# Optimization experiments

Measured on AMD Instinct MI355X. Metric: run time of the kernel, lower is better.

Reference implementation:

```python
import jax, jax.numpy as jnp
import numpy as np

TEMPERATURE = 0.1  # InfoNCE default
K_POS, K_NEG = 5, 10


def _l2norm(x, eps):
    return x / jnp.maximum(jnp.linalg.norm(x, axis=-1, keepdims=True), eps)


def setup_inputs() -> dict:
    key = jax.random.key(0)
    k1, k2 = jax.random.split(key)
    anchor = jax.random.normal(k1, (4096, 512), dtype=jnp.float32)
    sample = jax.random.normal(k2, (4096, 512), dtype=jnp.float32)
    return {"anchor": anchor, "sample": sample}


def reference(anchor, sample):
    N = anchor.shape[0]
    # Pairwise cosine similarity (torch.cosine_similarity eps=1e-8), computed
    a = _l2norm(anchor, 1e-8)
    sim = a @ a.T  # (N, N)

    # topk largest=True (5 nearest) and largest=False (10 farthest)
    _, pos_idx = jax.lax.top_k(sim, K_POS)    # (N, 5)
    _, neg_idx = jax.lax.top_k(-sim, K_NEG)   # (N, 10), ascending sim

    # Faithful replication of the original gather/repeat pattern:
    # query = sample.repeat(5, 1) -> tiling (index i maps to sample[i % N])
    query = jnp.tile(sample, (K_POS, 1))                          # (5N, d)
    pos = sample[pos_idx.reshape(-1)]                             # (5N, d) anchor-major
    neg = sample[neg_idx.reshape(-1)].reshape(N, K_NEG, -1)       # (N, 10, d)
    neg = jnp.repeat(neg, K_POS, axis=0)                          # (5N, 10, d)

    # InfoNCE (negative_mode='paired'): F.normalize (eps=1e-12) then logits.
    q = _l2norm(query, 1e-12)
    p = _l2norm(pos, 1e-12)
    n = _l2norm(neg, 1e-12)
    pos_logit = jnp.sum(q * p, axis=1, keepdims=True)             # (5N, 1)
    neg_logits = jnp.einsum('bd,bkd->bk', q, n)                   # (5N, 10)
    logits = jnp.concatenate([pos_logit, neg_logits], axis=1) / TEMPERATURE
    # cross_entropy with labels == 0, mean reduction
    loss = -jnp.mean(jax.nn.log_softmax(logits, axis=1)[:, 0])
    return loss
```

## Files before the change

### kernel.cpp

```cpp
#include <hip/hip_runtime.h>
#include <math.h>

#define N 4096
#define D 512
#define KPOS 5
#define KNEG 10
#define NB 32
#define NPAIR (NB * (NB - 1) / 2)
#define NJOB 1024

typedef short s16x8 __attribute__((ext_vector_type(8)));
typedef unsigned short u16x8 __attribute__((ext_vector_type(8)));
typedef float f32x4 __attribute__((ext_vector_type(4)));

__device__ __forceinline__ unsigned short f2bf(float x) {
    unsigned u = __float_as_uint(x);
    unsigned r = (u + 0x7FFFu + ((u >> 16) & 1u)) >> 16;
    return (unsigned short)r;
}
__device__ __forceinline__ float bf2f(unsigned short b) {
    return __uint_as_float(((unsigned)b) << 16);
}
__device__ __forceinline__ unsigned short mapbf(float x) {
    const unsigned short h = f2bf(x);
    return h ^ ((h & 0x8000u) ? 0xFFFFu : 0x8000u);
}
__device__ __forceinline__ unsigned umax_(unsigned a, unsigned b) { return a > b ? a : b; }
__device__ __forceinline__ unsigned umin_(unsigned a, unsigned b) { return a < b ? a : b; }

__global__ __launch_bounds__(256) void norm_kernel(const float* __restrict__ anchor,
                                                   const float* __restrict__ sample,
                                                   unsigned short* __restrict__ Abf,
                                                   unsigned short* __restrict__ s_norm) {
    const int wave = threadIdx.x >> 6, lane = threadIdx.x & 63;
    const int row = blockIdx.x * 4 + wave;
    const bool is_anchor = row < N;
    const float* in = is_anchor ? anchor + (size_t)row * D
                                : sample + (size_t)(row - N) * D;
    const float eps = is_anchor ? 1e-8f : 1e-12f;

    float v[8];
    float ss = 0.f;
#pragma unroll
    for (int e = 0; e < 8; ++e) {
        v[e] = in[lane + 64 * e];
        ss = fmaf(v[e], v[e], ss);
    }
#pragma unroll
    for (int off = 32; off > 0; off >>= 1) ss += __shfl_xor(ss, off);
    const float denom = fmaxf(sqrtf(ss), eps);

    unsigned short* out = is_anchor ? Abf + (size_t)row * D
                                    : s_norm + (size_t)(row - N) * D;
#pragma unroll
    for (int e = 0; e < 8; ++e) out[lane + 64 * e] = f2bf(v[e] / denom);
}

#define ATILE (128 * 64)
#define BTILE (64 * 64)

__device__ __forceinline__ void stage_ab(const unsigned short* __restrict__ A,
                                         unsigned short* As, unsigned short* Bs,
                                         int rowA, int colB, int kl, int t) {
#pragma unroll
    for (int i = 0; i < 4; ++i) {
        const int c = i * 256 + t;
        const int r = c >> 3;
        const int ke = ((c & 7) ^ (r & 7)) * 8;
        __builtin_amdgcn_global_load_lds(
            (const __attribute__((address_space(1))) void*)(A + (size_t)(rowA + r) * D + kl + ke),
            (__attribute__((address_space(3))) void*)(As + c * 8), 16, 0, 0);
    }
#pragma unroll
    for (int i = 0; i < 2; ++i) {
        const int c = i * 256 + t;
        const int r = c >> 3;
        const int ke = ((c & 7) ^ (r & 7)) * 8;
        __builtin_amdgcn_global_load_lds(
            (const __attribute__((address_space(1))) void*)(A + (size_t)(colB + r) * D + kl + ke),
            (__attribute__((address_space(3))) void*)(Bs + c * 8), 16, 0, 0);
    }
}

__global__ __launch_bounds__(256) void gemm_bf16(const unsigned short* __restrict__ Abf,
                                                 unsigned short* __restrict__ C) {
    const int q = (blockIdx.x % 8) * (NJOB / 8) + blockIdx.x / 8;

    int bi, bj, h;
    if (q < 2 * NPAIR) {
        const int op = q >> 1;
        h = q & 1;
        bi = (int)(31.5f - sqrtf(31.5f * 31.5f - 2.f * (float)op));
        while (31 * bi - bi * (bi - 1) / 2 > op) --bi;
        while (31 * (bi + 1) - (bi + 1) * bi / 2 <= op) ++bi;
        bj = bi + 1 + (op - (31 * bi - bi * (bi - 1) / 2));
    } else {
        const int d = q - 2 * NPAIR;
        bi = bj = d >> 1;
        h = d & 1;
    }

    __shared__ __align__(16) unsigned short As[2 * ATILE];
    __shared__ __align__(16) unsigned short Bs[2 * BTILE];

    const int t = threadIdx.x;
    const int l = t & 63;
    const int w = t >> 6;
    const int wr = w >> 1, wc = w & 1;
    const int rowA = bi * 128;
    const int colB = bj * 128 + h * 64;
    const int lrow = l & 15, lgrp = l >> 4;

    f32x4 acc[4][2];
#pragma unroll
    for (int m = 0; m < 4; ++m)
#pragma unroll
        for (int n = 0; n < 2; ++n) acc[m][n] = (f32x4){0.f, 0.f, 0.f, 0.f};

    stage_ab(Abf, As, Bs, rowA, colB, 0, t);
    __syncthreads();

    for (int kc = 0; kc < 8; ++kc) {
        const int cur = kc & 1;
        if (kc < 7)
            stage_ab(Abf, As + (cur ^ 1) * ATILE, Bs + (cur ^ 1) * BTILE,
                     rowA, colB, (kc + 1) * 64, t);

        const char* AsB = (const char*)(As + cur * ATILE);
        const char* BsB = (const char*)(Bs + cur * BTILE);
#pragma unroll
        for (int kk = 0; kk < 2; ++kk) {
            s16x8 af[4], bfr[2];
#pragma unroll
            for (int m = 0; m < 4; ++m) {
                const int row = wr * 64 + m * 16 + lrow;
                af[m] = *(const s16x8*)(AsB + row * 128 + (((kk * 4 + lgrp) ^ (row & 7)) * 16));
            }
#pragma unroll
            for (int n = 0; n < 2; ++n) {
                const int row = wc * 32 + n * 16 + lrow;
                bfr[n] = *(const s16x8*)(BsB + row * 128 + (((kk * 4 + lgrp) ^ (row & 7)) * 16));
            }
#pragma unroll
            for (int m = 0; m < 4; ++m)
#pragma unroll
                for (int n = 0; n < 2; ++n)
                    acc[m][n] = __builtin_amdgcn_mfma_f32_16x16x32_bf16(af[m], bfr[n], acc[m][n], 0, 0, 0);
        }
        __syncthreads();
    }

#pragma unroll
    for (int m = 0; m < 4; ++m) {
#pragma unroll
        for (int n = 0; n < 2; ++n) {
            const int col = colB + wc * 32 + n * 16 + lrow;
            const int row0 = rowA + wr * 64 + m * 16 + lgrp * 4;
#pragma unroll
            for (int j = 0; j < 4; ++j)
                C[(size_t)(row0 + j) * N + col] = mapbf(acc[m][n][j]);
        }
    }
    if (bi != bj) {
#pragma unroll
        for (int m = 0; m < 4; ++m) {
#pragma unroll
            for (int n = 0; n < 2; ++n) {
                const int col = colB + wc * 32 + n * 16 + lrow;
                const int row0 = rowA + wr * 64 + m * 16 + lgrp * 4;
                ushort4 pk;
                pk.x = mapbf(acc[m][n][0]);
                pk.y = mapbf(acc[m][n][1]);
                pk.z = mapbf(acc[m][n][2]);
                pk.w = mapbf(acc[m][n][3]);
                *(ushort4*)&C[(size_t)col * N + row0] = pk;
            }
        }
    }
}

__device__ __forceinline__ void ins_top(unsigned* tk, unsigned c) {
#pragma unroll
    for (int q = 0; q < KPOS - 1; ++q) {
        const unsigned x = umax_(tk[q], c);
        c = umin_(tk[q], c);
        tk[q] = x;
    }
    tk[KPOS - 1] = umax_(tk[KPOS - 1], c);
}
__device__ __forceinline__ void ins_bot(unsigned* bk, unsigned c) {
#pragma unroll
    for (int q = 0; q < KNEG - 1; ++q) {
        const unsigned x = umin_(bk[q], c);
        c = umax_(bk[q], c);
        bk[q] = x;
    }
    bk[KNEG - 1] = umin_(bk[KNEG - 1], c);
}
__device__ __forceinline__ void scan8(const unsigned short* __restrict__ s,
                                      int lane, int e, unsigned* tk, unsigned* bk) {
    const int base = 8 * (lane + 64 * e);
    const u16x8 v8 = *(const u16x8*)&s[base];
#pragma unroll
    for (int j = 0; j < 8; ++j) {
        const unsigned kv = ((unsigned)v8[j]) << 16;
        const int idx = base + j;
        ins_top(tk, kv | (unsigned)(idx ^ 0xFFF));
        ins_bot(bk, kv | (unsigned)idx);
    }
}

__global__ __launch_bounds__(256) void topk_kernel(const unsigned short* __restrict__ sim,
                                                   int* __restrict__ pos_idx,
                                                   int* __restrict__ neg_idx) {
    const int w = threadIdx.x >> 6, l = threadIdx.x & 63;
    const int row = blockIdx.x * 4 + w;
    const unsigned short* s = sim + (size_t)row * N;

    unsigned tkA[KPOS], bkA[KNEG], tkB[KPOS], bkB[KNEG];
#pragma unroll
    for (int q = 0; q < KPOS; ++q) { tkA[q] = 0u; tkB[q] = 0u; }
#pragma unroll
    for (int q = 0; q < KNEG; ++q) { bkA[q] = 0xFFFFFFFFu; bkB[q] = 0xFFFFFFFFu; }

#pragma unroll
    for (int ee = 0; ee < 4; ++ee) {
        scan8(s, l, 2 * ee, tkA, bkA);
        scan8(s, l, 2 * ee + 1, tkB, bkB);
    }
#pragma unroll
    for (int q = 0; q < KPOS; ++q) ins_top(tkA, tkB[q]);
#pragma unroll
    for (int q = 0; q < KNEG; ++q) ins_bot(bkA, bkB[q]);

#pragma unroll
    for (int it = 0; it < KPOS; ++it) {
        unsigned m = tkA[0];
#pragma unroll
        for (int off = 32; off > 0; off >>= 1) m = umax_(m, (unsigned)__shfl_xor((int)m, off));
        if (l == 0) pos_idx[row * KPOS + it] = (int)((m & 0xFFFu) ^ 0xFFFu);
        if (tkA[0] == m) {
#pragma unroll
            for (int q = 0; q < KPOS - 1; ++q) tkA[q] = tkA[q + 1];
            tkA[KPOS - 1] = 0u;
        }
    }
#pragma unroll
    for (int it = 0; it < KNEG; ++it) {
        unsigned m = bkA[0];
#pragma unroll
        for (int off = 32; off > 0; off >>= 1) m = umin_(m, (unsigned)__shfl_xor((int)m, off));
        if (l == 0) neg_idx[row * KNEG + it] = (int)(m & 0xFFFu);
        if (bkA[0] == m) {
#pragma unroll
            for (int q = 0; q < KNEG - 1; ++q) bkA[q] = bkA[q + 1];
            bkA[KNEG - 1] = 0xFFFFFFFFu;
        }
    }
}

__global__ __launch_bounds__(256) void loss_kernel(const unsigned short* __restrict__ s_norm,
                                                   const int* __restrict__ pos_idx,
                                                   const int* __restrict__ neg_idx,
                                                   float* __restrict__ partials) {
    __shared__ float wsum[4];
    const int wave = threadIdx.x >> 6, lane = threadIdx.x & 63;
    const int ia = blockIdx.x * 4 + wave;
    const int cc = lane & 15;
    const int g = lane >> 4;

    const int qbase = ia * KPOS;
    const int rowA = (qbase + ((cc < KPOS) ? cc : 0)) & (N - 1);
    int rowB;
    if (cc < KPOS)      rowB = pos_idx[qbase + cc];
    else if (cc < 15)   rowB = neg_idx[ia * KNEG + (cc - KPOS)];
    else                rowB = pos_idx[qbase];

    const unsigned short* pA = s_norm + (size_t)rowA * D + g * 8;
    const unsigned short* pB = s_norm + (size_t)rowB * D + g * 8;

    s16x8 a[16], b[16];
#pragma unroll
    for (int kk = 0; kk < 16; ++kk) {
        a[kk] = *(const s16x8*)(pA + kk * 32);
        b[kk] = *(const s16x8*)(pB + kk * 32);
    }
    __builtin_amdgcn_sched_barrier(0);
    asm volatile("" ::: "memory");

    f32x4 acc = (f32x4){0.f, 0.f, 0.f, 0.f};
#pragma unroll
    for (int kk = 0; kk < 16; ++kk)
        acc = __builtin_amdgcn_mfma_f32_16x16x32_bf16(a[kk], b[kk], acc, 0, 0, 0);

    float lsum = 0.f;
#pragma unroll
    for (int j = 0; j < 4; ++j) {
        const int p = g * 4 + j;
        const float logit = acc[j] * 10.f;
        const bool isneg = (cc >= KPOS) && (cc < 15);
        const bool ispos = (cc == p);
        float x = (ispos || isneg) ? logit : -__builtin_inff();
        float m = x;
#pragma unroll
        for (int off = 1; off < 16; off <<= 1) m = fmaxf(m, __shfl_xor(m, off));
        float e = (ispos || isneg) ? expf(logit - m) : 0.f;
        float sx = e;
#pragma unroll
        for (int off = 1; off < 16; off <<= 1) sx += __shfl_xor(sx, off);
        float l0 = ispos ? logit : 0.f;
#pragma unroll
        for (int off = 1; off < 16; off <<= 1) l0 += __shfl_xor(l0, off);
        if (p < KPOS && ispos) lsum += logf(sx) + m - l0;
    }

#pragma unroll
    for (int off = 32; off > 0; off >>= 1) lsum += __shfl_xor(lsum, off);
    if (lane == 0) wsum[wave] = lsum;
    __syncthreads();
    if (threadIdx.x == 0)
        partials[blockIdx.x] = wsum[0] + wsum[1] + wsum[2] + wsum[3];
}

__global__ __launch_bounds__(256) void reduce_kernel(const float* __restrict__ partials,
                                                     float* __restrict__ out) {
    __shared__ float wsum[4];
    const int wave = threadIdx.x >> 6, lane = threadIdx.x & 63;
    float s = partials[threadIdx.x] + partials[threadIdx.x + 256] +
              partials[threadIdx.x + 512] + partials[threadIdx.x + 768];
#pragma unroll
    for (int off = 32; off > 0; off >>= 1) s += __shfl_xor(s, off);
    if (lane == 0) wsum[wave] = s;
    __syncthreads();
    if (threadIdx.x == 0)
        *out = (wsum[0] + wsum[1] + wsum[2] + wsum[3]) * (1.0f / (float)(N * KPOS));
}

extern "C" void kernel_launch(void* const* d_in, const int* in_sizes, int n_in,
                              void* d_out, int out_size, void* d_ws, size_t ws_size,
                              hipStream_t stream) {
    const float* anchor = (const float*)d_in[0];
    const float* sample = (const float*)d_in[1];
    float* out = (float*)d_out;

    char* ws = (char*)d_ws;
    unsigned short* Abf    = (unsigned short*)ws;
    unsigned short* s_norm = (unsigned short*)(ws + (size_t)4 * 1024 * 1024);
    unsigned short* sim    = (unsigned short*)(ws + (size_t)8 * 1024 * 1024);
    int* pos_idx  = (int*)(ws + (size_t)40 * 1024 * 1024);
    int* neg_idx  = (int*)(ws + (size_t)40 * 1024 * 1024 + 128 * 1024);
    float* partials = (float*)(ws + (size_t)41 * 1024 * 1024);

    norm_kernel<<<2048, 256, 0, stream>>>(anchor, sample, Abf, s_norm);

    gemm_bf16<<<NJOB, 256, 0, stream>>>(Abf, sim);

    topk_kernel<<<N / 4, 256, 0, stream>>>(sim, pos_idx, neg_idx);

    loss_kernel<<<N / 4, 256, 0, stream>>>(s_norm, pos_idx, neg_idx, partials);

    reduce_kernel<<<1, 256, 0, stream>>>(partials, out);
}
```

Baseline: 71.01 us.

## Fuse top-k selection into loss kernel and vectorize normalization loads

Merges the top-k kernel and the loss kernel into one launch. Each wave finds its row's positive and negative indices with shuffles and hands them straight to the lanes that gather the sample rows, so the index arrays no longer go through global memory and one launch is removed. The normalization kernel also switches to float4 loads, ushort4 stores and a reciprocal multiply. The fused kernel holds more registers, which may reduce occupancy.

Measured after the change: 66.53 us. 6.3% less time.

```diff
diff --git a/kernel.cpp b/kernel.cpp
--- a/kernel.cpp
+++ b/kernel.cpp
@@ -39,21 +39,23 @@
                                 : sample + (size_t)(row - N) * D;
     const float eps = is_anchor ? 1e-8f : 1e-12f;
 
-    float v[8];
-    float ss = 0.f;
-#pragma unroll
-    for (int e = 0; e < 8; ++e) {
-        v[e] = in[lane + 64 * e];
-        ss = fmaf(v[e], v[e], ss);
-    }
+    const float4 v0 = *(const float4*)&in[lane * 4];
+    const float4 v1 = *(const float4*)&in[256 + lane * 4];
+    float ss = v0.x * v0.x + v0.y * v0.y + v0.z * v0.z + v0.w * v0.w
+             + v1.x * v1.x + v1.y * v1.y + v1.z * v1.z + v1.w * v1.w;
 #pragma unroll
     for (int off = 32; off > 0; off >>= 1) ss += __shfl_xor(ss, off);
-    const float denom = fmaxf(sqrtf(ss), eps);
+    const float inv = 1.0f / fmaxf(sqrtf(ss), eps);
 
     unsigned short* out = is_anchor ? Abf + (size_t)row * D
                                     : s_norm + (size_t)(row - N) * D;
-#pragma unroll
-    for (int e = 0; e < 8; ++e) out[lane + 64 * e] = f2bf(v[e] / denom);
+    ushort4 o0, o1;
+    o0.x = f2bf(v0.x * inv); o0.y = f2bf(v0.y * inv);
+    o0.z = f2bf(v0.z * inv); o0.w = f2bf(v0.w * inv);
+    o1.x = f2bf(v1.x * inv); o1.y = f2bf(v1.y * inv);
+    o1.z = f2bf(v1.z * inv); o1.w = f2bf(v1.w * inv);
+    *(ushort4*)&out[lane * 4] = o0;
+    *(ushort4*)&out[256 + lane * 4] = o1;
 }
 
 #define ATILE (128 * 64)
@@ -210,72 +212,59 @@
     }
 }
 
-__global__ __launch_bounds__(256) void topk_kernel(const unsigned short* __restrict__ sim,
-                                                   int* __restrict__ pos_idx,
-                                                   int* __restrict__ neg_idx) {
-    const int w = threadIdx.x >> 6, l = threadIdx.x & 63;
-    const int row = blockIdx.x * 4 + w;
-    const unsigned short* s = sim + (size_t)row * N;
-
-    unsigned tkA[KPOS], bkA[KNEG], tkB[KPOS], bkB[KNEG];
-#pragma unroll
-    for (int q = 0; q < KPOS; ++q) { tkA[q] = 0u; tkB[q] = 0u; }
-#pragma unroll
-    for (int q = 0; q < KNEG; ++q) { bkA[q] = 0xFFFFFFFFu; bkB[q] = 0xFFFFFFFFu; }
-
-#pragma unroll
-    for (int ee = 0; ee < 4; ++ee) {
-        scan8(s, l, 2 * ee, tkA, bkA);
-        scan8(s, l, 2 * ee + 1, tkB, bkB);
-    }
-#pragma unroll
-    for (int q = 0; q < KPOS; ++q) ins_top(tkA, tkB[q]);
-#pragma unroll
-    for (int q = 0; q < KNEG; ++q) ins_bot(bkA, bkB[q]);
-
-#pragma unroll
-    for (int it = 0; it < KPOS; ++it) {
-        unsigned m = tkA[0];
-#pragma unroll
-        for (int off = 32; off > 0; off >>= 1) m = umax_(m, (unsigned)__shfl_xor((int)m, off));
-        if (l == 0) pos_idx[row * KPOS + it] = (int)((m & 0xFFFu) ^ 0xFFFu);
-        if (tkA[0] == m) {
-#pragma unroll
-            for (int q = 0; q < KPOS - 1; ++q) tkA[q] = tkA[q + 1];
-            tkA[KPOS - 1] = 0u;
-        }
-    }
-#pragma unroll
-    for (int it = 0; it < KNEG; ++it) {
-        unsigned m = bkA[0];
-#pragma unroll
-        for (int off = 32; off > 0; off >>= 1) m = umin_(m, (unsigned)__shfl_xor((int)m, off));
-        if (l == 0) neg_idx[row * KNEG + it] = (int)(m & 0xFFFu);
-        if (bkA[0] == m) {
-#pragma unroll
-            for (int q = 0; q < KNEG - 1; ++q) bkA[q] = bkA[q + 1];
-            bkA[KNEG - 1] = 0xFFFFFFFFu;
-        }
-    }
-}
-
-__global__ __launch_bounds__(256) void loss_kernel(const unsigned short* __restrict__ s_norm,
-                                                   const int* __restrict__ pos_idx,
-                                                   const int* __restrict__ neg_idx,
-                                                   float* __restrict__ partials) {
+__global__ __launch_bounds__(256) void fused_topk_loss(const unsigned short* __restrict__ sim,
+                                                       const unsigned short* __restrict__ s_norm,
+                                                       float* __restrict__ partials) {
     __shared__ float wsum[4];
     const int wave = threadIdx.x >> 6, lane = threadIdx.x & 63;
     const int ia = blockIdx.x * 4 + wave;
+    const unsigned short* s = sim + (size_t)ia * N;
     const int cc = lane & 15;
     const int g = lane >> 4;
 
-    const int qbase = ia * KPOS;
-    const int rowA = (qbase + ((cc < KPOS) ? cc : 0)) & (N - 1);
-    int rowB;
-    if (cc < KPOS)      rowB = pos_idx[qbase + cc];
-    else if (cc < 15)   rowB = neg_idx[ia * KNEG + (cc - KPOS)];
-    else                rowB = pos_idx[qbase];
-
+    unsigned tkA[KPOS], bkA[KNEG], tkB[KPOS], bkB[KNEG];
+#pragma unroll
+    for (int q = 0; q < KPOS; ++q) { tkA[q] = 0u; tkB[q] = 0u; }
+#pragma unroll
+    for (int q = 0; q < KNEG; ++q) { bkA[q] = 0xFFFFFFFFu; bkB[q] = 0xFFFFFFFFu; }
+
+#pragma unroll
+    for (int ee = 0; ee < 4; ++ee) {
+        scan8(s, lane, 2 * ee, tkA, bkA);
+        scan8(s, lane, 2 * ee + 1, tkB, bkB);
+    }
+#pragma unroll
+    for (int q = 0; q < KPOS; ++q) ins_top(tkA, tkB[q]);
+#pragma unroll
+    for (int q = 0; q < KNEG; ++q) ins_bot(bkA, bkB[q]);
+
+    int rowB = 0;
+#pragma unroll
+    for (int it = 0; it < KPOS; ++it) {
+        unsigned m = tkA[0];
+#pragma unroll
+        for (int off = 32; off > 0; off >>= 1) m = umax_(m, (unsigned)__shfl_xor((int)m, off));
+        if (cc == it) rowB = (int)((m & 0xFFFu) ^ 0xFFFu);
+        if (tkA[0] == m) {
+#pragma unroll
+            for (int q = 0; q < KPOS - 1; ++q) tkA[q] = tkA[q + 1];
+            tkA[KPOS - 1] = 0u;
+        }
+    }
+#pragma unroll
+    for (int it = 0; it < KNEG; ++it) {
+        unsigned m = bkA[0];
+#pragma unroll
+        for (int off = 32; off > 0; off >>= 1) m = umin_(m, (unsigned)__shfl_xor((int)m, off));
+        if (cc == KPOS + it) rowB = (int)(m & 0xFFFu);
+        if (bkA[0] == m) {
+#pragma unroll
+            for (int q = 0; q < KNEG - 1; ++q) bkA[q] = bkA[q + 1];
+            bkA[KNEG - 1] = 0xFFFFFFFFu;
+        }
+    }
+
+    const int rowA = (ia * KPOS + ((cc < KPOS) ? cc : 0)) & (N - 1);
     const unsigned short* pA = s_norm + (size_t)rowA * D + g * 8;
     const unsigned short* pB = s_norm + (size_t)rowB * D + g * 8;
 
@@ -347,17 +336,13 @@
     unsigned short* Abf    = (unsigned short*)ws;
     unsigned short* s_norm = (unsigned short*)(ws + (size_t)4 * 1024 * 1024);
     unsigned short* sim    = (unsigned short*)(ws + (size_t)8 * 1024 * 1024);
-    int* pos_idx  = (int*)(ws + (size_t)40 * 1024 * 1024);
-    int* neg_idx  = (int*)(ws + (size_t)40 * 1024 * 1024 + 128 * 1024);
-    float* partials = (float*)(ws + (size_t)41 * 1024 * 1024);
+    float* partials = (float*)(ws + (size_t)40 * 1024 * 1024);
 
     norm_kernel<<<2048, 256, 0, stream>>>(anchor, sample, Abf, s_norm);
 
     gemm_bf16<<<NJOB, 256, 0, stream>>>(Abf, sim);
 
-    topk_kernel<<<N / 4, 256, 0, stream>>>(sim, pos_idx, neg_idx);
-
-    loss_kernel<<<N / 4, 256, 0, stream>>>(s_norm, pos_idx, neg_idx, partials);
+    fused_topk_loss<<<N / 4, 256, 0, stream>>>(sim, s_norm, partials);
 
     reduce_kernel<<<1, 256, 0, stream>>>(partials, out);
 }
```

## Split topk rows across two waves, vectorize norm, chunk loss loads

Applied to the files above, without the earlier changes.

The top-k kernel now gives each row to two waves, one per half of the row. Each wave prefetches its half into registers before scanning, and the two partial top/bottom lists are merged through LDS. This doubles the block count and shortens each wave's serial insertion chain. The norm kernel switches to float4 loads and ushort4 stores and multiplies by a reciprocal instead of dividing. The loss kernel loads operands in two chunks of eight to lower register pressure. The costs are a block-wide sync and a serial merge done by one lane.

Measured after the change: 71.98 us. About the same (+1.4%).

```diff
diff --git a/kernel.cpp b/kernel.cpp
--- a/kernel.cpp
+++ b/kernel.cpp
@@ -39,21 +39,23 @@
                                 : sample + (size_t)(row - N) * D;
     const float eps = is_anchor ? 1e-8f : 1e-12f;
 
-    float v[8];
-    float ss = 0.f;
-#pragma unroll
-    for (int e = 0; e < 8; ++e) {
-        v[e] = in[lane + 64 * e];
-        ss = fmaf(v[e], v[e], ss);
-    }
+    const float4 v0 = *(const float4*)&in[lane * 4];
+    const float4 v1 = *(const float4*)&in[256 + lane * 4];
+    float ss = v0.x * v0.x + v0.y * v0.y + v0.z * v0.z + v0.w * v0.w
+             + v1.x * v1.x + v1.y * v1.y + v1.z * v1.z + v1.w * v1.w;
 #pragma unroll
     for (int off = 32; off > 0; off >>= 1) ss += __shfl_xor(ss, off);
-    const float denom = fmaxf(sqrtf(ss), eps);
+    const float inv = 1.0f / fmaxf(sqrtf(ss), eps);
 
     unsigned short* out = is_anchor ? Abf + (size_t)row * D
                                     : s_norm + (size_t)(row - N) * D;
-#pragma unroll
-    for (int e = 0; e < 8; ++e) out[lane + 64 * e] = f2bf(v[e] / denom);
+    ushort4 o0, o1;
+    o0.x = f2bf(v0.x * inv); o0.y = f2bf(v0.y * inv);
+    o0.z = f2bf(v0.z * inv); o0.w = f2bf(v0.w * inv);
+    o1.x = f2bf(v1.x * inv); o1.y = f2bf(v1.y * inv);
+    o1.z = f2bf(v1.z * inv); o1.w = f2bf(v1.w * inv);
+    *(ushort4*)&out[lane * 4] = o0;
+    *(ushort4*)&out[256 + lane * 4] = o1;
 }
 
 #define ATILE (128 * 64)
@@ -197,10 +199,8 @@
     }
     bk[KNEG - 1] = umin_(bk[KNEG - 1], c);
 }
-__device__ __forceinline__ void scan8(const unsigned short* __restrict__ s,
-                                      int lane, int e, unsigned* tk, unsigned* bk) {
-    const int base = 8 * (lane + 64 * e);
-    const u16x8 v8 = *(const u16x8*)&s[base];
+__device__ __forceinline__ void scan_reg(const u16x8 v8, int base,
+                                         unsigned* tk, unsigned* bk) {
 #pragma unroll
     for (int j = 0; j < 8; ++j) {
         const unsigned kv = ((unsigned)v8[j]) << 16;
@@ -213,9 +213,20 @@
 __global__ __launch_bounds__(256) void topk_kernel(const unsigned short* __restrict__ sim,
                                                    int* __restrict__ pos_idx,
                                                    int* __restrict__ neg_idx) {
-    const int w = threadIdx.x >> 6, l = threadIdx.x & 63;
-    const int row = blockIdx.x * 4 + w;
-    const unsigned short* s = sim + (size_t)row * N;
+    __shared__ unsigned lds_top[4][KPOS];
+    __shared__ unsigned lds_bot[4][KNEG];
+    const int wave = threadIdx.x >> 6, lane = threadIdx.x & 63;
+    const int row = blockIdx.x * 2 + (wave >> 1);
+    const int half = wave & 1;
+    const unsigned short* srow = sim + (size_t)row * N;
+    const int hb = half * 2048;
+
+    u16x8 v0 = *(const u16x8*)&srow[hb + 8 * lane];
+    u16x8 v1 = *(const u16x8*)&srow[hb + 8 * (lane + 64)];
+    u16x8 v2 = *(const u16x8*)&srow[hb + 8 * (lane + 128)];
+    u16x8 v3 = *(const u16x8*)&srow[hb + 8 * (lane + 192)];
+    __builtin_amdgcn_sched_barrier(0);
+    asm volatile("" ::: "memory");
 
     unsigned tkA[KPOS], bkA[KNEG], tkB[KPOS], bkB[KNEG];
 #pragma unroll
@@ -223,22 +234,22 @@
 #pragma unroll
     for (int q = 0; q < KNEG; ++q) { bkA[q] = 0xFFFFFFFFu; bkB[q] = 0xFFFFFFFFu; }
 
-#pragma unroll
-    for (int ee = 0; ee < 4; ++ee) {
-        scan8(s, l, 2 * ee, tkA, bkA);
-        scan8(s, l, 2 * ee + 1, tkB, bkB);
-    }
+    scan_reg(v0, hb + 8 * lane,         tkA, bkA);
+    scan_reg(v1, hb + 8 * (lane + 64),  tkB, bkB);
+    scan_reg(v2, hb + 8 * (lane + 128), tkA, bkA);
+    scan_reg(v3, hb + 8 * (lane + 192), tkB, bkB);
 #pragma unroll
     for (int q = 0; q < KPOS; ++q) ins_top(tkA, tkB[q]);
 #pragma unroll
     for (int q = 0; q < KNEG; ++q) ins_bot(bkA, bkB[q]);
 
+    unsigned wt[KPOS], wb[KNEG];
 #pragma unroll
     for (int it = 0; it < KPOS; ++it) {
         unsigned m = tkA[0];
 #pragma unroll
         for (int off = 32; off > 0; off >>= 1) m = umax_(m, (unsigned)__shfl_xor((int)m, off));
-        if (l == 0) pos_idx[row * KPOS + it] = (int)((m & 0xFFFu) ^ 0xFFFu);
+        wt[it] = m;
         if (tkA[0] == m) {
 #pragma unroll
             for (int q = 0; q < KPOS - 1; ++q) tkA[q] = tkA[q + 1];
@@ -250,12 +261,30 @@
         unsigned m = bkA[0];
 #pragma unroll
         for (int off = 32; off > 0; off >>= 1) m = umin_(m, (unsigned)__shfl_xor((int)m, off));
-        if (l == 0) neg_idx[row * KNEG + it] = (int)(m & 0xFFFu);
+        wb[it] = m;
         if (bkA[0] == m) {
 #pragma unroll
             for (int q = 0; q < KNEG - 1; ++q) bkA[q] = bkA[q + 1];
             bkA[KNEG - 1] = 0xFFFFFFFFu;
         }
+    }
+
+    if (half == 1 && lane == 0) {
+#pragma unroll
+        for (int i = 0; i < KPOS; ++i) lds_top[wave][i] = wt[i];
+#pragma unroll
+        for (int i = 0; i < KNEG; ++i) lds_bot[wave][i] = wb[i];
+    }
+    __syncthreads();
+    if (half == 0 && lane == 0) {
+#pragma unroll
+        for (int i = 0; i < KPOS; ++i) ins_top(wt, lds_top[wave + 1][i]);
+#pragma unroll
+        for (int i = 0; i < KNEG; ++i) ins_bot(wb, lds_bot[wave + 1][i]);
+#pragma unroll
+        for (int i = 0; i < KPOS; ++i) pos_idx[row * KPOS + i] = (int)((wt[i] & 0xFFFu) ^ 0xFFFu);
+#pragma unroll
+        for (int i = 0; i < KNEG; ++i) neg_idx[row * KNEG + i] = (int)(wb[i] & 0xFFFu);
     }
 }
 
@@ -279,19 +308,21 @@
     const unsigned short* pA = s_norm + (size_t)rowA * D + g * 8;
     const unsigned short* pB = s_norm + (size_t)rowB * D + g * 8;
 
-    s16x8 a[16], b[16];
-#pragma unroll
-    for (int kk = 0; kk < 16; ++kk) {
-        a[kk] = *(const s16x8*)(pA + kk * 32);
-        b[kk] = *(const s16x8*)(pB + kk * 32);
-    }
-    __builtin_amdgcn_sched_barrier(0);
-    asm volatile("" ::: "memory");
-
     f32x4 acc = (f32x4){0.f, 0.f, 0.f, 0.f};
 #pragma unroll
-    for (int kk = 0; kk < 16; ++kk)
-        acc = __builtin_amdgcn_mfma_f32_16x16x32_bf16(a[kk], b[kk], acc, 0, 0, 0);
+    for (int ch = 0; ch < 2; ++ch) {
+        s16x8 a[8], b[8];
+#pragma unroll
+        for (int kk = 0; kk < 8; ++kk) {
+            a[kk] = *(const s16x8*)(pA + (ch * 8 + kk) * 32);
+            b[kk] = *(const s16x8*)(pB + (ch * 8 + kk) * 32);
+        }
+        __builtin_amdgcn_sched_barrier(0);
+        asm volatile("" ::: "memory");
+#pragma unroll
+        for (int kk = 0; kk < 8; ++kk)
+            acc = __builtin_amdgcn_mfma_f32_16x16x32_bf16(a[kk], b[kk], acc, 0, 0, 0);
+    }
 
     float lsum = 0.f;
 #pragma unroll
@@ -355,7 +386,7 @@
 
     gemm_bf16<<<NJOB, 256, 0, stream>>>(Abf, sim);
 
-    topk_kernel<<<N / 4, 256, 0, stream>>>(sim, pos_idx, neg_idx);
+    topk_kernel<<<N / 2, 256, 0, stream>>>(sim, pos_idx, neg_idx);
 
     loss_kernel<<<N / 4, 256, 0, stream>>>(s_norm, pos_idx, neg_idx, partials);
 
```
